# Kernel tuning notes

Measured on AMD Instinct MI355X. Metric: run time of the kernel, lower is better.

Reference implementation:

```python
import jax, jax.numpy as jnp
import numpy as np

DIM = 2048
MLP_MULT = 4
NUM_EXPERTS = 8
EXPERT_INTER = MLP_MULT * DIM // NUM_EXPERTS  # 1024
B, S = 4, 2048


def setup_inputs() -> dict:
    key = jax.random.key(0)
    k1, k2, k3, k4 = jax.random.split(key, 4)
    x = jax.random.normal(k1, (B, S, DIM), dtype=jnp.float32)
    expert_ids = jax.random.randint(k2, (B, S), 0, NUM_EXPERTS, dtype=jnp.int64)
    # kaiming-uniform-ish scale for gate_up; down_proj random (zeros in orig init
    # would make output trivially zero, unhelpful for a correctness baseline)
    bound_gu = float(np.sqrt(1.0 / DIM))
    gate_up_proj = jax.random.uniform(k3, (NUM_EXPERTS, DIM, 2 * EXPERT_INTER),
                                      dtype=jnp.float32, minval=-bound_gu, maxval=bound_gu)
    bound_dn = float(np.sqrt(1.0 / EXPERT_INTER))
    down_proj = jax.random.uniform(k4, (NUM_EXPERTS, EXPERT_INTER, DIM),
                                   dtype=jnp.float32, minval=-bound_dn, maxval=bound_dn)
    return {"x": x, "expert_ids": expert_ids,
            "gate_up_proj": gate_up_proj, "down_proj": down_proj}


def reference(x, expert_ids, gate_up_proj, down_proj):
    Bb, Ss, D = x.shape
    E = gate_up_proj.shape[0]
    flat_x = x.reshape(-1, D)            # [T, D], T = B*S
    flat_ids = expert_ids.reshape(-1)    # [T]
    # Same math as the torch loop: full dense per-expert MLP, then mask.
    gu = jnp.einsum('td,edh->eth', flat_x, gate_up_proj)       # [E, T, 2I]
    g, u = jnp.split(gu, 2, axis=-1)                           # [E, T, I] each
    h = jax.nn.silu(g) * u                                     # [E, T, I]
    y = jnp.einsum('eti,eid->etd', h, down_proj)               # [E, T, D]
    mask = (flat_ids[None, :] == jnp.arange(E)[:, None])[..., None]  # [E, T, 1]
    out = jnp.sum(y * mask.astype(y.dtype), axis=0)            # [T, D]
    return out.reshape(Bb, Ss, D)
```

## Files before the change

### kernel.cpp

```cpp
#include <hip/hip_runtime.h>
#include <cstdint>
#include <cstddef>


typedef __attribute__((ext_vector_type(8))) _Float16 half8;
typedef __attribute__((ext_vector_type(4))) _Float16 half4;
typedef __attribute__((ext_vector_type(4))) float floatx4;

#define AS_G __attribute__((address_space(1)))
#define AS_L __attribute__((address_space(3)))

__device__ __forceinline__ void async_cp16(void* lds, const void* g) {
  __builtin_amdgcn_global_load_lds((const AS_G uint32_t*)g, (AS_L uint32_t*)lds,
                                   16, 0, 0);
}

static constexpr int TTOK = 8192;
static constexpr int DIMK = 2048;
static constexpr int EI = 1024;
static constexpr int NE = 8;
static constexpr int PADT = 9216;
static constexpr int MAXTILES = 80;
static constexpr int NTILE_LAUNCH = 72;

__global__ __launch_bounds__(256) void k_route(const int* __restrict__ ids,
                                               int* __restrict__ perm,
                                               int* __restrict__ te,
                                               int* __restrict__ tr0,
                                               int* __restrict__ tnr) {
  __shared__ int cnt[NE];
  __shared__ int cur[NE];
  int tid = threadIdx.x;
  if (tid < NE) cnt[tid] = 0;
  __syncthreads();
  for (int t = tid; t < TTOK; t += 256) atomicAdd(&cnt[ids[t]], 1);
  __syncthreads();
  if (tid == 0) {
    int pr = 0, nt = 0;
    for (int e = 0; e < NE; e++) {
      int n = cnt[e];
      cur[e] = pr;
      for (int j = 0; j < n; j += 128) {
        te[nt] = e; tr0[nt] = pr + j; tnr[nt] = min(128, n - j); nt++;
      }
      pr += ((n + 127) >> 7) << 7;
    }
    for (; nt < MAXTILES; nt++) { te[nt] = 0; tr0[nt] = 0; tnr[nt] = 0; }
  }
  __syncthreads();
  for (int i = tid; i < PADT; i += 256) perm[i] = 0;
  __syncthreads();
  for (int t = tid; t < TTOK; t += 256) {
    int p = atomicAdd(&cur[ids[t]], 1);
    perm[p] = t;
  }
}

template <int K, int N>
__global__ __launch_bounds__(256) void k_transpose_cvt(
    const float* __restrict__ src, _Float16* __restrict__ dst) {
  __shared__ float tile[64][67];
  int e = blockIdx.z;
  int n0 = blockIdx.x * 64, k0 = blockIdx.y * 64;
  const float* s = src + (size_t)e * K * N;
  _Float16* d = dst + (size_t)e * N * K;
  int tid = threadIdx.x;
  int kk = tid >> 4;
  int nn = (tid & 15) * 4;
#pragma unroll
  for (int i = 0; i < 4; i++) {
    float4 v = *(const float4*)(s + (size_t)(k0 + kk + i * 16) * N + n0 + nn);
    tile[kk + i * 16][nn + 0] = v.x;
    tile[kk + i * 16][nn + 1] = v.y;
    tile[kk + i * 16][nn + 2] = v.z;
    tile[kk + i * 16][nn + 3] = v.w;
  }
  __syncthreads();
  int nr = tid >> 4;
  int k4 = (tid & 15) * 4;
#pragma unroll
  for (int i = 0; i < 4; i++) {
    int n = nr + i * 16;
    half4 o;
    o[0] = (_Float16)tile[k4 + 0][n];
    o[1] = (_Float16)tile[k4 + 1][n];
    o[2] = (_Float16)tile[k4 + 2][n];
    o[3] = (_Float16)tile[k4 + 3][n];
    *(half4*)(d + (size_t)(n0 + n) * K + k0 + k4) = o;
  }
}

__global__ __launch_bounds__(256) void k_gateup(
    const float* __restrict__ x, const _Float16* __restrict__ wt1,
    const int* __restrict__ perm, const int* __restrict__ te,
    const int* __restrict__ tr0, const int* __restrict__ tnr,
    _Float16* __restrict__ hbuf) {
  int tile = blockIdx.y;
  int nr = tnr[tile];
  if (nr == 0) return;
  int e = te[tile], r0 = tr0[tile];
  int col = blockIdx.x * 64;
  int tid = threadIdx.x;

  __shared__ __align__(16) _Float16 As[128 * 32];
  __shared__ __align__(16) _Float16 Bg[64 * 32];
  __shared__ __align__(16) _Float16 Bu[64 * 32];

  int arow = tid >> 1, ah = tid & 1;
  const float* aptr = x + (size_t)perm[r0 + arow] * DIMK + ah * 16;
  int asw = (arow >> 1) & 3;
  _Float16* aw0 = As + ((size_t)arow * 4 + ((2 * ah) ^ asw)) * 8;
  _Float16* aw1 = As + ((size_t)arow * 4 + ((2 * ah + 1) ^ asw)) * 8;

  int bn = tid >> 2;
  int bq = (tid & 3) ^ ((tid >> 3) & 3);
  const _Float16* bgp =
      wt1 + (size_t)e * DIMK * DIMK + (size_t)(col + bn) * DIMK + bq * 8;
  const _Float16* bup = bgp + (size_t)EI * DIMK;
  _Float16* bgl = Bg + (size_t)tid * 8;
  _Float16* bul = Bu + (size_t)tid * 8;

  int wave = tid >> 6, lane = tid & 63;
  int wm = (wave & 1) * 64, wn = (wave >> 1) * 32;
  int lm = lane & 15, lq = lane >> 4;
  int aoff[4], boff[2];
#pragma unroll
  for (int i = 0; i < 4; i++) {
    int r = wm + i * 16 + lm;
    aoff[i] = (r * 4 + (lq ^ ((r >> 1) & 3))) * 8;
  }
#pragma unroll
  for (int j = 0; j < 2; j++) {
    int n = wn + j * 16 + lm;
    boff[j] = (n * 4 + (lq ^ ((n >> 1) & 3))) * 8;
  }

  floatx4 accg[4][2], accu[4][2];
#pragma unroll
  for (int i = 0; i < 4; i++)
#pragma unroll
    for (int j = 0; j < 2; j++) {
      accg[i][j] = (floatx4)0.0f;
      accu[i][j] = (floatx4)0.0f;
    }

  for (int k0 = 0; k0 < DIMK; k0 += 32) {
    async_cp16(bgl, bgp + k0);
    async_cp16(bul, bup + k0);
    float4 f0 = *(const float4*)(aptr + k0);
    float4 f1 = *(const float4*)(aptr + k0 + 4);
    float4 f2 = *(const float4*)(aptr + k0 + 8);
    float4 f3 = *(const float4*)(aptr + k0 + 12);
    half8 p0, p1;
    p0[0] = (_Float16)f0.x; p0[1] = (_Float16)f0.y;
    p0[2] = (_Float16)f0.z; p0[3] = (_Float16)f0.w;
    p0[4] = (_Float16)f1.x; p0[5] = (_Float16)f1.y;
    p0[6] = (_Float16)f1.z; p0[7] = (_Float16)f1.w;
    p1[0] = (_Float16)f2.x; p1[1] = (_Float16)f2.y;
    p1[2] = (_Float16)f2.z; p1[3] = (_Float16)f2.w;
    p1[4] = (_Float16)f3.x; p1[5] = (_Float16)f3.y;
    p1[6] = (_Float16)f3.z; p1[7] = (_Float16)f3.w;
    *(half8*)aw0 = p0;
    *(half8*)aw1 = p1;
    __syncthreads();

    half8 af[4], bgf[2], buf_[2];
#pragma unroll
    for (int i = 0; i < 4; i++) af[i] = *(const half8*)(As + aoff[i]);
#pragma unroll
    for (int j = 0; j < 2; j++) {
      bgf[j] = *(const half8*)(Bg + boff[j]);
      buf_[j] = *(const half8*)(Bu + boff[j]);
    }
#pragma unroll
    for (int i = 0; i < 4; i++)
#pragma unroll
      for (int j = 0; j < 2; j++) {
        accg[i][j] = __builtin_amdgcn_mfma_f32_16x16x32_f16(af[i], bgf[j],
                                                            accg[i][j], 0, 0, 0);
        accu[i][j] = __builtin_amdgcn_mfma_f32_16x16x32_f16(af[i], buf_[j],
                                                            accu[i][j], 0, 0, 0);
      }
    __syncthreads();
  }

#pragma unroll
  for (int i = 0; i < 4; i++) {
    int rbase = wm + i * 16 + lq * 4;
#pragma unroll
    for (int j = 0; j < 2; j++) {
      int c = col + wn + j * 16 + lm;
#pragma unroll
      for (int rr = 0; rr < 4; rr++) {
        float g = accg[i][j][rr];
        float u = accu[i][j][rr];
        float h = g / (1.0f + __expf(-g)) * u;
        hbuf[(size_t)(r0 + rbase + rr) * EI + c] = (_Float16)h;
      }
    }
  }
}

__global__ __launch_bounds__(256) void k_down(
    const _Float16* __restrict__ hbuf, const _Float16* __restrict__ wt2,
    const int* __restrict__ perm, const int* __restrict__ te,
    const int* __restrict__ tr0, const int* __restrict__ tnr,
    float* __restrict__ out) {
  int tile = blockIdx.y;
  int nr = tnr[tile];
  if (nr == 0) return;
  int e = te[tile], r0 = tr0[tile];
  int col = blockIdx.x * 128;
  int tid = threadIdx.x;

  __shared__ __align__(16) _Float16 As[128 * 32];
  __shared__ __align__(16) _Float16 Bs[128 * 32];

  int an = tid >> 2;
  int aq = (tid & 3) ^ ((tid >> 3) & 3);
  const _Float16* ap0 = hbuf + (size_t)(r0 + an) * EI + aq * 8;
  const _Float16* ap1 = hbuf + (size_t)(r0 + 64 + an) * EI + aq * 8;
  _Float16* al0 = As + (size_t)tid * 8;
  _Float16* al1 = As + 2048 + (size_t)tid * 8;
  const _Float16* wte = wt2 + (size_t)e * DIMK * EI;
  const _Float16* bp0 = wte + (size_t)(col + an) * EI + aq * 8;
  const _Float16* bp1 = wte + (size_t)(col + 64 + an) * EI + aq * 8;
  _Float16* bl0 = Bs + (size_t)tid * 8;
  _Float16* bl1 = Bs + 2048 + (size_t)tid * 8;

  int wave = tid >> 6, lane = tid & 63;
  int wm = (wave & 1) * 64, wn = (wave >> 1) * 64;
  int lm = lane & 15, lq = lane >> 4;
  int aoff[4], boff[4];
#pragma unroll
  for (int i = 0; i < 4; i++) {
    int r = wm + i * 16 + lm;
    aoff[i] = (r * 4 + (lq ^ ((r >> 1) & 3))) * 8;
    int n = wn + i * 16 + lm;
    boff[i] = (n * 4 + (lq ^ ((n >> 1) & 3))) * 8;
  }

  floatx4 acc[4][4];
#pragma unroll
  for (int i = 0; i < 4; i++)
#pragma unroll
    for (int j = 0; j < 4; j++) acc[i][j] = (floatx4)0.0f;

  for (int k0 = 0; k0 < EI; k0 += 32) {
    async_cp16(al0, ap0 + k0);
    async_cp16(al1, ap1 + k0);
    async_cp16(bl0, bp0 + k0);
    async_cp16(bl1, bp1 + k0);
    __syncthreads();
    half8 af[4], bf[4];
#pragma unroll
    for (int i = 0; i < 4; i++) {
      af[i] = *(const half8*)(As + aoff[i]);
      bf[i] = *(const half8*)(Bs + boff[i]);
    }
#pragma unroll
    for (int i = 0; i < 4; i++)
#pragma unroll
      for (int j = 0; j < 4; j++)
        acc[i][j] =
            __builtin_amdgcn_mfma_f32_16x16x32_f16(af[i], bf[j], acc[i][j], 0, 0, 0);
    __syncthreads();
  }

#pragma unroll
  for (int i = 0; i < 4; i++) {
    int rbase = wm + i * 16 + lq * 4;
#pragma unroll
    for (int rr = 0; rr < 4; rr++) {
      int r = rbase + rr;
      if (r < nr) {
        int tok = perm[r0 + r];
        float* orow = out + (size_t)tok * DIMK + col;
#pragma unroll
        for (int j = 0; j < 4; j++) orow[wn + j * 16 + lm] = acc[i][j][rr];
      }
    }
  }
}

extern "C" void kernel_launch(void* const* d_in, const int* in_sizes, int n_in,
                              void* d_out, int out_size, void* d_ws,
                              size_t ws_size, hipStream_t stream) {
  const float* x = (const float*)d_in[0];
  const int* ids = (const int*)d_in[1];
  const float* gup = (const float*)d_in[2];
  const float* dwn = (const float*)d_in[3];
  float* out = (float*)d_out;
  char* ws = (char*)d_ws;

  int* perm = (int*)ws;
  int* te = (int*)(ws + 36864);
  int* tr0 = (int*)(ws + 36864 + 512);
  int* tnr = (int*)(ws + 36864 + 1024);
  _Float16* wt1 = (_Float16*)(ws + 65536);
  _Float16* wt2 = (_Float16*)(ws + 65536 + 67108864);
  _Float16* hbuf = (_Float16*)(ws + 65536 + 67108864 + 33554432);

  k_route<<<dim3(1), dim3(256), 0, stream>>>(ids, perm, te, tr0, tnr);
  k_transpose_cvt<2048, 2048>
      <<<dim3(32, 32, 8), dim3(256), 0, stream>>>(gup, wt1);
  k_transpose_cvt<1024, 2048>
      <<<dim3(32, 16, 8), dim3(256), 0, stream>>>(dwn, wt2);
  k_gateup<<<dim3(16, NTILE_LAUNCH), dim3(256), 0, stream>>>(
      x, wt1, perm, te, tr0, tnr, hbuf);
  k_down<<<dim3(16, NTILE_LAUNCH), dim3(256), 0, stream>>>(
      hbuf, wt2, perm, te, tr0, tnr, out);
}
```

Measured before the change: 569.5 us.

## Pre-gather tokens to fp16 and load A tiles asynchronously in gate-up GEMM

Adds a gather kernel that permutes token rows and converts them to fp16 once. The gate-up GEMM can then stream A tiles with async global-to-LDS copies instead of doing per-iteration fp32 loads, conversion and LDS stores. It also widens the transpose-convert stores to 8 halves and reorders launches so the down-proj weights reuse the gate-up weight buffer, shrinking the workspace. The cost is an extra kernel pass over x, and the A-tile LDS layout and swizzle change.

```diff
diff --git a/kernel.cpp b/kernel.cpp
--- a/kernel.cpp
+++ b/kernel.cpp
@@ -4,7 +4,6 @@
 
 
 typedef __attribute__((ext_vector_type(8))) _Float16 half8;
-typedef __attribute__((ext_vector_type(4))) _Float16 half4;
 typedef __attribute__((ext_vector_type(4))) float floatx4;
 
 #define AS_G __attribute__((address_space(1)))
@@ -54,6 +53,23 @@
     int p = atomicAdd(&cur[ids[t]], 1);
     perm[p] = t;
   }
+}
+
+__global__ __launch_bounds__(256) void k_gather_cvt(
+    const float* __restrict__ x, const int* __restrict__ perm,
+    _Float16* __restrict__ xg) {
+  int r = blockIdx.x;
+  int tok = perm[r];
+  int c = threadIdx.x * 8;
+  const float* s = x + (size_t)tok * DIMK + c;
+  float4 a = *(const float4*)s;
+  float4 b = *(const float4*)(s + 4);
+  half8 o;
+  o[0] = (_Float16)a.x; o[1] = (_Float16)a.y;
+  o[2] = (_Float16)a.z; o[3] = (_Float16)a.w;
+  o[4] = (_Float16)b.x; o[5] = (_Float16)b.y;
+  o[6] = (_Float16)b.z; o[7] = (_Float16)b.w;
+  *(half8*)(xg + (size_t)r * DIMK + c) = o;
 }
 
 template <int K, int N>
@@ -76,25 +92,22 @@
     tile[kk + i * 16][nn + 3] = v.w;
   }
   __syncthreads();
-  int nr = tid >> 4;
-  int k4 = (tid & 15) * 4;
-#pragma unroll
-  for (int i = 0; i < 4; i++) {
-    int n = nr + i * 16;
-    half4 o;
-    o[0] = (_Float16)tile[k4 + 0][n];
-    o[1] = (_Float16)tile[k4 + 1][n];
-    o[2] = (_Float16)tile[k4 + 2][n];
-    o[3] = (_Float16)tile[k4 + 3][n];
-    *(half4*)(d + (size_t)(n0 + n) * K + k0 + k4) = o;
+  int nrow = tid >> 3;
+  int k8 = (tid & 7) * 8;
+#pragma unroll
+  for (int i = 0; i < 2; i++) {
+    int n = nrow + i * 32;
+    half8 o;
+#pragma unroll
+    for (int j = 0; j < 8; j++) o[j] = (_Float16)tile[k8 + j][n];
+    *(half8*)(d + (size_t)(n0 + n) * K + k0 + k8) = o;
   }
 }
 
 __global__ __launch_bounds__(256) void k_gateup(
-    const float* __restrict__ x, const _Float16* __restrict__ wt1,
-    const int* __restrict__ perm, const int* __restrict__ te,
-    const int* __restrict__ tr0, const int* __restrict__ tnr,
-    _Float16* __restrict__ hbuf) {
+    const _Float16* __restrict__ xg, const _Float16* __restrict__ wt1,
+    const int* __restrict__ te, const int* __restrict__ tr0,
+    const int* __restrict__ tnr, _Float16* __restrict__ hbuf) {
   int tile = blockIdx.y;
   int nr = tnr[tile];
   if (nr == 0) return;
@@ -106,11 +119,12 @@
   __shared__ __align__(16) _Float16 Bg[64 * 32];
   __shared__ __align__(16) _Float16 Bu[64 * 32];
 
-  int arow = tid >> 1, ah = tid & 1;
-  const float* aptr = x + (size_t)perm[r0 + arow] * DIMK + ah * 16;
-  int asw = (arow >> 1) & 3;
-  _Float16* aw0 = As + ((size_t)arow * 4 + ((2 * ah) ^ asw)) * 8;
-  _Float16* aw1 = As + ((size_t)arow * 4 + ((2 * ah + 1) ^ asw)) * 8;
+  int an = tid >> 2;
+  int aq = (tid & 3) ^ ((tid >> 3) & 3);
+  const _Float16* ap0 = xg + (size_t)(r0 + an) * DIMK + aq * 8;
+  const _Float16* ap1 = xg + (size_t)(r0 + 64 + an) * DIMK + aq * 8;
+  _Float16* al0 = As + (size_t)tid * 8;
+  _Float16* al1 = As + 2048 + (size_t)tid * 8;
 
   int bn = tid >> 2;
   int bq = (tid & 3) ^ ((tid >> 3) & 3);
@@ -145,25 +159,11 @@
     }
 
   for (int k0 = 0; k0 < DIMK; k0 += 32) {
+    async_cp16(al0, ap0 + k0);
+    async_cp16(al1, ap1 + k0);
     async_cp16(bgl, bgp + k0);
     async_cp16(bul, bup + k0);
-    float4 f0 = *(const float4*)(aptr + k0);
-    float4 f1 = *(const float4*)(aptr + k0 + 4);
-    float4 f2 = *(const float4*)(aptr + k0 + 8);
-    float4 f3 = *(const float4*)(aptr + k0 + 12);
-    half8 p0, p1;
-    p0[0] = (_Float16)f0.x; p0[1] = (_Float16)f0.y;
-    p0[2] = (_Float16)f0.z; p0[3] = (_Float16)f0.w;
-    p0[4] = (_Float16)f1.x; p0[5] = (_Float16)f1.y;
-    p0[6] = (_Float16)f1.z; p0[7] = (_Float16)f1.w;
-    p1[0] = (_Float16)f2.x; p1[1] = (_Float16)f2.y;
-    p1[2] = (_Float16)f2.z; p1[3] = (_Float16)f2.w;
-    p1[4] = (_Float16)f3.x; p1[5] = (_Float16)f3.y;
-    p1[6] = (_Float16)f3.z; p1[7] = (_Float16)f3.w;
-    *(half8*)aw0 = p0;
-    *(half8*)aw1 = p1;
     __syncthreads();
-
     half8 af[4], bgf[2], buf_[2];
 #pragma unroll
     for (int i = 0; i < 4; i++) af[i] = *(const half8*)(As + aoff[i]);
@@ -298,16 +298,18 @@
   int* tr0 = (int*)(ws + 36864 + 512);
   int* tnr = (int*)(ws + 36864 + 1024);
   _Float16* wt1 = (_Float16*)(ws + 65536);
-  _Float16* wt2 = (_Float16*)(ws + 65536 + 67108864);
-  _Float16* hbuf = (_Float16*)(ws + 65536 + 67108864 + 33554432);
+  _Float16* hbuf = (_Float16*)(ws + 65536 + 67108864);
+  _Float16* xg = (_Float16*)(ws + 65536 + 67108864 + 18874368);
+  _Float16* wt2 = wt1;
 
   k_route<<<dim3(1), dim3(256), 0, stream>>>(ids, perm, te, tr0, tnr);
+  k_gather_cvt<<<dim3(PADT), dim3(256), 0, stream>>>(x, perm, xg);
   k_transpose_cvt<2048, 2048>
       <<<dim3(32, 32, 8), dim3(256), 0, stream>>>(gup, wt1);
+  k_gateup<<<dim3(16, NTILE_LAUNCH), dim3(256), 0, stream>>>(
+      xg, wt1, te, tr0, tnr, hbuf);
   k_transpose_cvt<1024, 2048>
       <<<dim3(32, 16, 8), dim3(256), 0, stream>>>(dwn, wt2);
-  k_gateup<<<dim3(16, NTILE_LAUNCH), dim3(256), 0, stream>>>(
-      x, wt1, perm, te, tr0, tnr, hbuf);
   k_down<<<dim3(16, NTILE_LAUNCH), dim3(256), 0, stream>>>(
       hbuf, wt2, perm, te, tr0, tnr, out);
 }
```

Measured after the change: 520.3 us. 8.6% less time.
